# Kernel tuning notes

Hardware: AMD Instinct MI355X
Metric: run time of the kernel (lower is better)

## Reference

```python
import jax, jax.numpy as jnp
import numpy as np

NQ = 7  # start_qubits
QCSTEP = [4, 1, 2, 1, 1, 1]


def _ry(psi, theta, w):
    """Apply RY(theta) on wire w. psi: [B] + [2]*NQ, wire w at axis w+1."""
    ax = w + 1
    c = jnp.cos(theta / 2)
    s = jnp.sin(theta / 2)
    a0 = jax.lax.index_in_dim(psi, 0, ax, keepdims=False)
    a1 = jax.lax.index_in_dim(psi, 1, ax, keepdims=False)
    return jnp.stack([c * a0 - s * a1, s * a0 + c * a1], axis=ax)


def _cnot(psi, c, t):
    """Apply CNOT(control=c, target=t)."""
    axc, axt = c + 1, t + 1
    s0 = jax.lax.index_in_dim(psi, 0, axc, keepdims=False)
    s1 = jax.lax.index_in_dim(psi, 1, axc, keepdims=False)
    axt2 = axt if axt < axc else axt - 1  # target axis after removing control axis
    s1 = jnp.flip(s1, axis=axt2)
    return jnp.stack([s0, s1], axis=axc)


def _simulate(x, QCs, QPs, QF):
    B = x.shape[0]
    # AmplitudeEmbedding with normalize=True (real input -> real state, wire 0 = MSB)
    psi = x / jnp.linalg.norm(x, axis=1, keepdims=True)
    psi = psi.reshape((B,) + (2,) * NQ)
    for j in range(6):
        sq = NQ - j
        qc, qp, step = QCs[j], QPs[j], QCSTEP[j]
        idx = 0
        for i in range(sq):
            psi = _ry(psi, qc[idx], i); idx += 1
        for i in range(sq):
            if i == 0:
                psi = _ry(psi, qc[idx], 0); idx += 1
                psi = _cnot(psi, sq - 1, 0)
                psi = _ry(psi, qc[idx], 0); idx += 1
            else:
                w = sq - i
                psi = _ry(psi, qc[idx], w); idx += 1
                psi = _cnot(psi, w - 1, w)
                psi = _ry(psi, qc[idx], w); idx += 1
        for i in range(sq):
            psi = _ry(psi, qc[idx], i); idx += 1
        control, controled = 0, step
        for i in range(sq):
            psi = _ry(psi, qc[idx], controled); idx += 1
            psi = _cnot(psi, control, controled)
            psi = _ry(psi, qc[idx], controled); idx += 1
            control = controled
            controled = (controled + step) % sq
        pidx = 0
        for i in range(sq - 1):
            psi = _ry(psi, qp[pidx], i + 1); pidx += 1
            psi = _cnot(psi, i, i + 1)
            psi = _ry(psi, qp[pidx], i + 1); pidx += 1
    psi = _ry(psi, QF[0], 0)
    # probs on wire 0: marginalize amplitudes^2 over wires 1..6 -> [B, 2]
    return jnp.sum(psi * psi, axis=tuple(range(2, NQ + 1)))


def setup_inputs() -> dict:
    key = jax.random.key(0)
    ks = jax.random.split(key, 15)
    B = 262144
    inp = {"x": jax.random.normal(ks[0], (B, 2 ** NQ), dtype=jnp.float32)}
    qc_sizes = [42, 36, 30, 24, 18, 12]
    qp_sizes = [12, 10, 8, 6, 4, 2]
    for j in range(6):
        inp[f"QC{j + 1}"] = jax.random.normal(ks[1 + j], (qc_sizes[j],), dtype=jnp.float32)
        inp[f"QP{j + 1}"] = jax.random.normal(ks[7 + j], (qp_sizes[j],), dtype=jnp.float32)
    inp["QF"] = jax.random.normal(ks[13], (1,), dtype=jnp.float32)
    return inp


def reference(x, QC1, QC2, QC3, QC4, QC5, QC6, QP1, QP2, QP3, QP4, QP5, QP6, QF):
    QCs = [QC1, QC2, QC3, QC4, QC5, QC6]
    QPs = [QP1, QP2, QP3, QP4, QP5, QP6]
    return _simulate(x, QCs, QPs, QF)
```

## Files before the change

kernel.cpp:

```cpp
#include <hip/hip_runtime.h>

typedef _Float16 f16x8 __attribute__((ext_vector_type(8)));
typedef float f32x4 __attribute__((ext_vector_type(4)));


__device__ __forceinline__ void ry_gate(float& a0, float& a1, int w, int lane,
                                        float c, float s) {
  if (w == 0) {
    float n0 = c * a0 - s * a1;
    float n1 = s * a0 + c * a1;
    a0 = n0; a1 = n1;
  } else {
    int m = 1 << (6 - w);
    float p0 = __shfl_xor(a0, m);
    float p1 = __shfl_xor(a1, m);
    if (lane & m) {
      a0 = s * p0 + c * a0;
      a1 = s * p1 + c * a1;
    } else {
      a0 = c * a0 - s * p0;
      a1 = c * a1 - s * p1;
    }
  }
}

__device__ __forceinline__ void cnot_gate(float& a0, float& a1, int c, int t,
                                          int lane) {
  if (c == 0) {
    int mt = 1 << (6 - t);
    a1 = __shfl_xor(a1, mt);
  } else if (t == 0) {
    int mc = 1 << (6 - c);
    if (lane & mc) { float tmp = a0; a0 = a1; a1 = tmp; }
  } else {
    int mc = 1 << (6 - c), mt = 1 << (6 - t);
    float p0 = __shfl_xor(a0, mt);
    float p1 = __shfl_xor(a1, mt);
    if (lane & mc) { a0 = p0; a1 = p1; }
  }
}

__global__ __launch_bounds__(64) void basis_kernel(
    const float* __restrict__ qc1, const float* __restrict__ qc2,
    const float* __restrict__ qc3, const float* __restrict__ qc4,
    const float* __restrict__ qc5, const float* __restrict__ qc6,
    const float* __restrict__ qp1, const float* __restrict__ qp2,
    const float* __restrict__ qp3, const float* __restrict__ qp4,
    const float* __restrict__ qp5, const float* __restrict__ qp6,
    const float* __restrict__ qf, _Float16* __restrict__ wt) {
  __shared__ float2 cs[208];
  int lane = threadIdx.x;

  {
    const float* arrs[13] = {qc1, qp1, qc2, qp2, qc3, qp3, qc4,
                             qp4, qc5, qp5, qc6, qp6, qf};
    const int sizes[13] = {42, 12, 36, 10, 30, 8, 24, 6, 18, 4, 12, 2, 1};
    for (int t = lane; t < 205; t += 64) {
      int base = 0; float ang = 0.f;
#pragma unroll
      for (int s2 = 0; s2 < 13; ++s2) {
        if (t >= base && t < base + sizes[s2]) ang = arrs[s2][t - base];
        base += sizes[s2];
      }
      float h = 0.5f * ang;
      cs[t] = make_float2(cosf(h), sinf(h));
    }
  }
  __syncthreads();

  int k = blockIdx.x;
  float a0 = ((k >> 6) == 0 && (k & 63) == lane) ? 1.0f : 0.0f;
  float a1 = ((k >> 6) == 1 && (k & 63) == lane) ? 1.0f : 0.0f;
  int g = 0;

  const int qcstep[6] = {4, 1, 2, 1, 1, 1};
#define RYG(w)                                        \
  { float2 csv = cs[g++]; ry_gate(a0, a1, (w), lane, csv.x, csv.y); }
#define CNG(c, t) cnot_gate(a0, a1, (c), (t), lane);

#pragma unroll
  for (int j = 0; j < 6; ++j) {
    int sq = 7 - j;
    int step = qcstep[j];
    for (int i = 0; i < sq; ++i) { RYG(i); }
    for (int i = 0; i < sq; ++i) {
      if (i == 0) { RYG(0); CNG(sq - 1, 0); RYG(0); }
      else { int w = sq - i; RYG(w); CNG(w - 1, w); RYG(w); }
    }
    for (int i = 0; i < sq; ++i) { RYG(i); }
    int control = 0, controled = step;
    for (int i = 0; i < sq; ++i) {
      RYG(controled); CNG(control, controled); RYG(controled);
      control = controled; controled = (controled + step) % sq;
    }
    for (int i = 0; i < sq - 1; ++i) { RYG(i + 1); CNG(i, i + 1); RYG(i + 1); }
  }
  RYG(0);

  {
    int ks = k >> 5, khi = (k >> 3) & 3, j = k & 7;
    int nf0 = lane >> 4, lr = lane & 15;
    wt[(ks * 8 + nf0) * 512 + khi * 128 + lr * 8 + j] = (_Float16)a0;
    wt[(ks * 8 + nf0 + 4) * 512 + khi * 128 + lr * 8 + j] = (_Float16)a1;
  }
#undef RYG
#undef CNG
}

__global__ __launch_bounds__(256, 4) void qcnn_gemm(
    const float* __restrict__ X, const _Float16* __restrict__ wt,
    float* __restrict__ out, int M) {
  __shared__ uint4 ldsbuf[2048];
  int tid = threadIdx.x;
  int wave = tid >> 6, lane = tid & 63;
  int lr = lane & 15;
  int g = lane >> 4;
  int lk = g * 8;

  size_t base0 = (size_t)blockIdx.x * 256 + wave * 16;

  float4 v0[4], v1[4];
  if (base0 < (size_t)M) {
    const float* xp = X + (base0 + lr) * 128 + lk;
#pragma unroll
    for (int ks = 0; ks < 4; ++ks) {
      v0[ks] = *(const float4*)(xp + ks * 32);
      v1[ks] = *(const float4*)(xp + ks * 32 + 4);
    }
  }

  {
    const uint4* wv = (const uint4*)wt;
#pragma unroll
    for (int c = 0; c < 8; ++c) ldsbuf[c * 256 + tid] = wv[c * 256 + tid];
  }
  __syncthreads();

  const char* bbase = (const char*)ldsbuf + lane * 16;

#pragma unroll
  for (int t = 0; t < 4; ++t) {
    size_t rb = base0 + (size_t)t * 64;
    if (rb < (size_t)M) {
      f16x8 a[4];
#pragma unroll
      for (int ks = 0; ks < 4; ++ks) {
        auto p0 = __builtin_amdgcn_cvt_pkrtz(v0[ks].x, v0[ks].y);
        auto p1 = __builtin_amdgcn_cvt_pkrtz(v0[ks].z, v0[ks].w);
        auto p2 = __builtin_amdgcn_cvt_pkrtz(v1[ks].x, v1[ks].y);
        auto p3 = __builtin_amdgcn_cvt_pkrtz(v1[ks].z, v1[ks].w);
        f16x8 f;
        f[0] = (_Float16)p0[0]; f[1] = (_Float16)p0[1];
        f[2] = (_Float16)p1[0]; f[3] = (_Float16)p1[1];
        f[4] = (_Float16)p2[0]; f[5] = (_Float16)p2[1];
        f[6] = (_Float16)p3[0]; f[7] = (_Float16)p3[1];
        a[ks] = f;
      }

      if (t < 3) {
        size_t rn = base0 + (size_t)(t + 1) * 64;
        if (rn < (size_t)M) {
          const float* xp = X + (rn + lr) * 128 + lk;
#pragma unroll
          for (int ks = 0; ks < 4; ++ks) {
            v0[ks] = *(const float4*)(xp + ks * 32);
            v1[ks] = *(const float4*)(xp + ks * 32 + 4);
          }
        }
      }

      f32x4 acc[8];
#pragma unroll
      for (int nf = 0; nf < 8; ++nf) acc[nf] = (f32x4){0.f, 0.f, 0.f, 0.f};

#pragma unroll
      for (int ks = 0; ks < 4; ++ks) {
#pragma unroll
        for (int nf = 0; nf < 8; ++nf) {
          f16x8 b = *(const f16x8*)(bbase + (ks * 8 + nf) * 1024);
          acc[nf] = __builtin_amdgcn_mfma_f32_16x16x32_f16(a[ks], b, acc[nf], 0, 0, 0);
        }
      }

      float s0[4], s1[4];
#pragma unroll
      for (int r = 0; r < 4; ++r) {
        float t0 = 0.f, t1 = 0.f;
#pragma unroll
        for (int nf = 0; nf < 4; ++nf) t0 += acc[nf][r] * acc[nf][r];
#pragma unroll
        for (int nf = 4; nf < 8; ++nf) t1 += acc[nf][r] * acc[nf][r];
        s0[r] = t0; s1[r] = t1;
      }
#pragma unroll
      for (int d = 1; d < 16; d <<= 1) {
#pragma unroll
        for (int r = 0; r < 4; ++r) {
          s0[r] += __shfl_xor(s0[r], d);
          s1[r] += __shfl_xor(s1[r], d);
        }
      }
      size_t row = rb + g * 4;
#pragma unroll
      for (int r = 0; r < 4; ++r) {
        if ((lane & 15) == r) {
          float inv = 1.0f / (s0[r] + s1[r]);
          *(float2*)(out + (row + r) * 2) =
              make_float2(s0[r] * inv, s1[r] * inv);
        }
      }
    }
  }
}

extern "C" void kernel_launch(void* const* d_in, const int* in_sizes, int n_in,
                              void* d_out, int out_size, void* d_ws,
                              size_t ws_size, hipStream_t stream) {
  const float* X = (const float*)d_in[0];
  _Float16* wt = (_Float16*)d_ws;

  basis_kernel<<<128, 64, 0, stream>>>(
       (const float*)d_in[1],  (const float*)d_in[3],
       (const float*)d_in[5],  (const float*)d_in[7],
       (const float*)d_in[9],  (const float*)d_in[11],
       (const float*)d_in[2],  (const float*)d_in[4],
       (const float*)d_in[6],  (const float*)d_in[8],
       (const float*)d_in[10],  (const float*)d_in[12],
       (const float*)d_in[13], wt);

  int M = in_sizes[0] / 128;
  int nblk = (M + 255) / 256;
  qcnn_gemm<<<nblk, 256, 0, stream>>>(X, wt, (float*)d_out, M);
}
```

Baseline: 42.26 us.

## Fuse basis simulation into GEMM kernel with global flag synchronization

Merges the circuit-basis kernel into the GEMM kernel. The first 128 blocks each simulate one basis column, write it to the workspace and bump an atomic counter, and every block spin-waits until the counter reaches 128 before loading the weights. This removes a separate launch and the gap between the two kernels, overlapping the X prefetch with basis construction. It adds a memset launch and relies on the first 128 blocks being resident or scheduled first, which risks a deadlock or stalls if scheduling order differs.

```diff
diff --git a/kernel.cpp b/kernel.cpp
--- a/kernel.cpp
+++ b/kernel.cpp
@@ -40,75 +40,16 @@
   }
 }
 
-__global__ __launch_bounds__(64) void basis_kernel(
+__global__ __launch_bounds__(256, 4) void fused_qcnn(
+    const float* __restrict__ X,
     const float* __restrict__ qc1, const float* __restrict__ qc2,
     const float* __restrict__ qc3, const float* __restrict__ qc4,
     const float* __restrict__ qc5, const float* __restrict__ qc6,
     const float* __restrict__ qp1, const float* __restrict__ qp2,
     const float* __restrict__ qp3, const float* __restrict__ qp4,
     const float* __restrict__ qp5, const float* __restrict__ qp6,
-    const float* __restrict__ qf, _Float16* __restrict__ wt) {
-  __shared__ float2 cs[208];
-  int lane = threadIdx.x;
-
-  {
-    const float* arrs[13] = {qc1, qp1, qc2, qp2, qc3, qp3, qc4,
-                             qp4, qc5, qp5, qc6, qp6, qf};
-    const int sizes[13] = {42, 12, 36, 10, 30, 8, 24, 6, 18, 4, 12, 2, 1};
-    for (int t = lane; t < 205; t += 64) {
-      int base = 0; float ang = 0.f;
-#pragma unroll
-      for (int s2 = 0; s2 < 13; ++s2) {
-        if (t >= base && t < base + sizes[s2]) ang = arrs[s2][t - base];
-        base += sizes[s2];
-      }
-      float h = 0.5f * ang;
-      cs[t] = make_float2(cosf(h), sinf(h));
-    }
-  }
-  __syncthreads();
-
-  int k = blockIdx.x;
-  float a0 = ((k >> 6) == 0 && (k & 63) == lane) ? 1.0f : 0.0f;
-  float a1 = ((k >> 6) == 1 && (k & 63) == lane) ? 1.0f : 0.0f;
-  int g = 0;
-
-  const int qcstep[6] = {4, 1, 2, 1, 1, 1};
-#define RYG(w)                                        \
-  { float2 csv = cs[g++]; ry_gate(a0, a1, (w), lane, csv.x, csv.y); }
-#define CNG(c, t) cnot_gate(a0, a1, (c), (t), lane);
-
-#pragma unroll
-  for (int j = 0; j < 6; ++j) {
-    int sq = 7 - j;
-    int step = qcstep[j];
-    for (int i = 0; i < sq; ++i) { RYG(i); }
-    for (int i = 0; i < sq; ++i) {
-      if (i == 0) { RYG(0); CNG(sq - 1, 0); RYG(0); }
-      else { int w = sq - i; RYG(w); CNG(w - 1, w); RYG(w); }
-    }
-    for (int i = 0; i < sq; ++i) { RYG(i); }
-    int control = 0, controled = step;
-    for (int i = 0; i < sq; ++i) {
-      RYG(controled); CNG(control, controled); RYG(controled);
-      control = controled; controled = (controled + step) % sq;
-    }
-    for (int i = 0; i < sq - 1; ++i) { RYG(i + 1); CNG(i, i + 1); RYG(i + 1); }
-  }
-  RYG(0);
-
-  {
-    int ks = k >> 5, khi = (k >> 3) & 3, j = k & 7;
-    int nf0 = lane >> 4, lr = lane & 15;
-    wt[(ks * 8 + nf0) * 512 + khi * 128 + lr * 8 + j] = (_Float16)a0;
-    wt[(ks * 8 + nf0 + 4) * 512 + khi * 128 + lr * 8 + j] = (_Float16)a1;
-  }
-#undef RYG
-#undef CNG
-}
-
-__global__ __launch_bounds__(256, 4) void qcnn_gemm(
-    const float* __restrict__ X, const _Float16* __restrict__ wt,
+    const float* __restrict__ qf,
+    _Float16* __restrict__ wt, unsigned* __restrict__ flag,
     float* __restrict__ out, int M) {
   __shared__ uint4 ldsbuf[2048];
   int tid = threadIdx.x;
@@ -128,6 +69,73 @@
       v1[ks] = *(const float4*)(xp + ks * 32 + 4);
     }
   }
+
+  if (blockIdx.x < 128) {
+    float2* cs = (float2*)ldsbuf;
+    {
+      const float* arrs[13] = {qc1, qp1, qc2, qp2, qc3, qp3, qc4,
+                               qp4, qc5, qp5, qc6, qp6, qf};
+      const int sizes[13] = {42, 12, 36, 10, 30, 8, 24, 6, 18, 4, 12, 2, 1};
+      for (int t = tid; t < 205; t += 256) {
+        int base = 0; float ang = 0.f;
+#pragma unroll
+        for (int s2 = 0; s2 < 13; ++s2) {
+          if (t >= base && t < base + sizes[s2]) ang = arrs[s2][t - base];
+          base += sizes[s2];
+        }
+        float h = 0.5f * ang;
+        cs[t] = make_float2(cosf(h), sinf(h));
+      }
+    }
+    __syncthreads();
+
+    if (wave == 0) {
+      int k = blockIdx.x;
+      float a0 = ((k >> 6) == 0 && (k & 63) == lane) ? 1.0f : 0.0f;
+      float a1 = ((k >> 6) == 1 && (k & 63) == lane) ? 1.0f : 0.0f;
+      int gi = 0;
+
+      const int qcstep[6] = {4, 1, 2, 1, 1, 1};
+#define RYG(w)                                        \
+  { float2 csv = cs[gi++]; ry_gate(a0, a1, (w), lane, csv.x, csv.y); }
+#define CNG(c, t) cnot_gate(a0, a1, (c), (t), lane);
+
+#pragma unroll
+      for (int j = 0; j < 6; ++j) {
+        int sq = 7 - j;
+        int step = qcstep[j];
+        for (int i = 0; i < sq; ++i) { RYG(i); }
+        for (int i = 0; i < sq; ++i) {
+          if (i == 0) { RYG(0); CNG(sq - 1, 0); RYG(0); }
+          else { int w = sq - i; RYG(w); CNG(w - 1, w); RYG(w); }
+        }
+        for (int i = 0; i < sq; ++i) { RYG(i); }
+        int control = 0, controled = step;
+        for (int i = 0; i < sq; ++i) {
+          RYG(controled); CNG(control, controled); RYG(controled);
+          control = controled; controled = (controled + step) % sq;
+        }
+        for (int i = 0; i < sq - 1; ++i) { RYG(i + 1); CNG(i, i + 1); RYG(i + 1); }
+      }
+      RYG(0);
+#undef RYG
+#undef CNG
+
+      int ks = k >> 5, khi = (k >> 3) & 3, j = k & 7;
+      int nf0 = lane >> 4, lr0 = lane & 15;
+      wt[(ks * 8 + nf0) * 512 + khi * 128 + lr0 * 8 + j] = (_Float16)a0;
+      wt[(ks * 8 + nf0 + 4) * 512 + khi * 128 + lr0 * 8 + j] = (_Float16)a1;
+      __threadfence();
+      if (lane == 0) atomicAdd(flag, 1u);
+    }
+    __syncthreads();
+  }
+
+  if (tid == 0) {
+    while (atomicAdd(flag, 0u) < 128u) __builtin_amdgcn_s_sleep(8);
+  }
+  __syncthreads();
+  __threadfence();
 
   {
     const uint4* wv = (const uint4*)wt;
@@ -218,17 +226,20 @@
                               size_t ws_size, hipStream_t stream) {
   const float* X = (const float*)d_in[0];
   _Float16* wt = (_Float16*)d_ws;
-
-  basis_kernel<<<128, 64, 0, stream>>>(
+  unsigned* flag = (unsigned*)((char*)d_ws + 32768);
+
+  hipMemsetAsync(flag, 0, sizeof(unsigned), stream);
+
+  int M = in_sizes[0] / 128;
+  int nblk = (M + 255) / 256;
+
+  fused_qcnn<<<nblk, 256, 0, stream>>>(
+      X,
        (const float*)d_in[1],  (const float*)d_in[3],
        (const float*)d_in[5],  (const float*)d_in[7],
        (const float*)d_in[9],  (const float*)d_in[11],
        (const float*)d_in[2],  (const float*)d_in[4],
        (const float*)d_in[6],  (const float*)d_in[8],
        (const float*)d_in[10],  (const float*)d_in[12],
-       (const float*)d_in[13], wt);
-
-  int M = in_sizes[0] / 128;
-  int nblk = (M + 255) / 256;
-  qcnn_gemm<<<nblk, 256, 0, stream>>>(X, wt, (float*)d_out, M);
-}
+       (const float*)d_in[13], wt, flag, (float*)d_out, M);
+}
```

New measurement: 115.7 us. +173.9%, slower.
